# Kernel optimization log

Measured on AMD Instinct MI355X. Metric: run time of the kernel, lower is better.

Reference implementation:

```python
import jax, jax.numpy as jnp
import numpy as np

N = 100000
D = 128
E = 1600000
NEG_SLOPE = 0.2


def gatv2_layer(x, src, dst, Wl, Wr, att, b):
    # GATv2Conv (heads=1, eval mode): lin_l -> source/message feats, lin_r -> target feats
    xl = x @ Wl                      # [N, D]
    xr = x @ Wr                      # [N, D]
    # per-edge score: a^T LeakyReLU(x_l[src] + x_r[dst])
    z = jax.nn.leaky_relu(xl[src] + xr[dst], NEG_SLOPE)  # [E, D]
    e = z @ att                      # [E]
    # segment softmax over incoming edges of each dst node
    m = jax.ops.segment_max(e, dst, num_segments=N)      # [N]
    ex = jnp.exp(e - m[dst])
    s = jax.ops.segment_sum(ex, dst, num_segments=N)     # [N]
    alpha = ex / (s[dst] + 1e-16)                        # [E]
    # weighted scatter-aggregate of source messages
    out = jax.ops.segment_sum(alpha[:, None] * xl[src], dst, num_segments=N)
    return out + b


def setup_inputs() -> dict:
    key = jax.random.key(0)
    ks = jax.random.split(key, 6)
    scale = 1.0 / np.sqrt(D)
    x = jax.random.normal(ks[0], (N, D), dtype=jnp.float32)
    edge_index = jax.random.randint(ks[1], (2, E), 0, N, dtype=jnp.int64)
    Wl = jax.random.normal(ks[2], (3, D, D), dtype=jnp.float32) * scale
    Wr = jax.random.normal(ks[3], (3, D, D), dtype=jnp.float32) * scale
    att = jax.random.normal(ks[4], (3, D), dtype=jnp.float32) * scale
    b = jax.random.normal(ks[5], (3, D), dtype=jnp.float32) * 0.01
    return {"x": x, "Wl": Wl, "Wr": Wr, "att": att, "b": b, "edge_index": edge_index}


def reference(x, Wl, Wr, att, b, edge_index):
    src, dst = edge_index[0], edge_index[1]
    h = gatv2_layer(x, src, dst, Wl[0], Wr[0], att[0], b[0])
    h = jax.nn.relu(h)
    h = gatv2_layer(h, src, dst, Wl[1], Wr[1], att[1], b[1])
    h = jax.nn.relu(h)
    h = gatv2_layer(h, src, dst, Wl[2], Wr[2], att[2], b[2])
    return h
```

## Files before the change

kernel.cpp:

```cpp
#include <hip/hip_runtime.h>
#include <math.h>

#define DD 128
#define NEG 0.2f

typedef short short8 __attribute__((ext_vector_type(8)));
typedef float f32x4 __attribute__((ext_vector_type(4)));
typedef float f32x2 __attribute__((ext_vector_type(2)));
typedef _Float16 h2v __attribute__((ext_vector_type(2)));

__device__ __forceinline__ unsigned short f2bf(float f) {
    unsigned u = __float_as_uint(f);
    return (unsigned short)((u + 0x7fffu + ((u >> 16) & 1u)) >> 16);
}
__device__ __forceinline__ float bf2f(unsigned short h) {
    return __uint_as_float(((unsigned)h) << 16);
}

#if __has_builtin(__builtin_amdgcn_exp2f)
#define EXP2F(x) __builtin_amdgcn_exp2f(x)
#else
#define EXP2F(x) exp2f(x)
#endif

__device__ void excl_scan_1024(int* sh, int* aux) {
    __syncthreads();
    int t = threadIdx.x;
    int base = t * 4;
    int a0 = sh[base], a1 = sh[base + 1], a2 = sh[base + 2], a3 = sh[base + 3];
    int s = a0 + a1 + a2 + a3;
    aux[t] = s;
    __syncthreads();
    for (int off = 1; off < 256; off <<= 1) {
        int v = (t >= off) ? aux[t - off] : 0;
        __syncthreads();
        aux[t] += v;
        __syncthreads();
    }
    int excl = aux[t] - s;
    sh[base] = excl;
    sh[base + 1] = excl + a0;
    sh[base + 2] = excl + a0 + a1;
    sh[base + 3] = excl + a0 + a1 + a2;
    __syncthreads();
}

__global__ __launch_bounds__(256) void k_histC(const int* __restrict__ dst,
                                               int* __restrict__ histC, int E, int CB) {
    __shared__ int h[1024];
    int t = threadIdx.x;
    for (int j = t; j < 1024; j += 256) h[j] = 0;
    __syncthreads();
    int stride = gridDim.x * 256;
    for (int i = blockIdx.x * 256 + t; i < E; i += stride)
        atomicAdd(&h[dst[i] >> 7], 1);
    __syncthreads();
    for (int j = t; j < CB; j += 256)
        if (h[j]) atomicAdd(&histC[j], h[j]);
}

__global__ __launch_bounds__(256) void k_scanC2(const int* __restrict__ histC,
                                                int* __restrict__ baseC,
                                                int* __restrict__ cursorC, int CB) {
    __shared__ int sh[1024];
    __shared__ int aux[256];
    int t = threadIdx.x;
    for (int j = t; j < 1024; j += 256) sh[j] = (j < CB) ? histC[j] : 0;
    excl_scan_1024(sh, aux);
    for (int j = t; j <= CB; j += 256) {
        baseC[j] = sh[j];
        if (j < CB) cursorC[j] = sh[j];
    }
}

#define CHUNK 8192
__global__ __launch_bounds__(256) void k_part3(const int* __restrict__ srcI,
                                               const int* __restrict__ dstI,
                                               int* __restrict__ cursorC,
                                               uint2* __restrict__ part,
                                               int E, int CB) {
    __shared__ int sh[1024];
    __shared__ int aux[256];
    __shared__ int resBase[1024];
    __shared__ int cur[1024];
    __shared__ uint2 stage[CHUNK];
    int t = threadIdx.x;
    int c0 = blockIdx.x * CHUNK;
    int cnt = E - c0; if (cnt > CHUNK) cnt = CHUNK;

    for (int j = t; j < 1024; j += 256) sh[j] = 0;
    __syncthreads();
    for (int i = t; i < cnt; i += 256)
        atomicAdd(&sh[dstI[c0 + i] >> 7], 1);
    __syncthreads();
    for (int j = t; j < CB; j += 256) {
        int c = sh[j];
        resBase[j] = c ? atomicAdd(&cursorC[j], c) : 0;
    }
    excl_scan_1024(sh, aux);
    for (int j = t; j < 1024; j += 256) cur[j] = sh[j];
    __syncthreads();
    for (int i = t; i < cnt; i += 256) {
        unsigned s = (unsigned)srcI[c0 + i];
        unsigned d = (unsigned)dstI[c0 + i];
        int b = (int)(d >> 7);
        int pos = atomicAdd(&cur[b], 1);
        stage[pos].x = s;
        stage[pos].y = d;
    }
    __syncthreads();
    for (int i = t; i < cnt; i += 256) {
        uint2 v = stage[i];
        int b = (int)(v.y >> 7);
        part[resBase[b] + (i - sh[b])] = v;
    }
}

__global__ __launch_bounds__(256) void k_part4(const uint2* __restrict__ part,
                                               const int* __restrict__ baseC,
                                               int* __restrict__ srcs,
                                               int* __restrict__ row_ptr,
                                               int N) {
    __shared__ int hist[128];
    __shared__ int incl[128];
    __shared__ int cur[128];
    __shared__ unsigned srcS[8192];
    int b = blockIdx.x;
    int t = threadIdx.x;
    int base = baseC[b];
    int cnt = baseC[b + 1] - base;
    int node0 = b << 7;

    if (t < 128) hist[t] = 0;
    __syncthreads();
    for (int i = t; i < cnt; i += 256)
        atomicAdd(&hist[part[base + i].y & 127], 1);
    __syncthreads();
    if (t < 128) incl[t] = hist[t];
    __syncthreads();
    for (int off = 1; off < 128; off <<= 1) {
        int v = 0;
        if (t < 128 && t >= off) v = incl[t - off];
        __syncthreads();
        if (t < 128) incl[t] += v;
        __syncthreads();
    }
    if (t < 128) cur[t] = incl[t] - hist[t];
    __syncthreads();
    for (int i = t; i < cnt; i += 256) {
        uint2 e = part[base + i];
        int r = atomicAdd(&cur[e.y & 127], 1);
        if (r < 8192) srcS[r] = e.x;
    }
    __syncthreads();
    for (int i = t; i < cnt; i += 256)
        srcs[base + i] = (int)srcS[i];
    int nodes = N - node0; if (nodes > 128) nodes = 128;
    if (t < nodes) row_ptr[node0 + t + 1] = base + incl[t];
    if (b == 0 && t == 0) row_ptr[0] = 0;
}

#define NCH 8192
__global__ __launch_bounds__(256) void k_deghist(const int* __restrict__ row_ptr,
                                                 int* __restrict__ histD, int N) {
    __shared__ int h[128];
    int t = threadIdx.x;
    if (t < 128) h[t] = 0;
    __syncthreads();
    int c0 = blockIdx.x * NCH;
    int cnt = N - c0; if (cnt > NCH) cnt = NCH;
    for (int i = t; i < cnt; i += 256) {
        int deg = row_ptr[c0 + i + 1] - row_ptr[c0 + i];
        int c = deg < 127 ? deg : 127;
        atomicAdd(&h[c], 1);
    }
    __syncthreads();
    if (t < 128 && h[t]) atomicAdd(&histD[t], h[t]);
}

__global__ __launch_bounds__(128) void k_degscan(const int* __restrict__ histD,
                                                 int* __restrict__ cursorD) {
    __shared__ int sh[128];
    int t = threadIdx.x;
    int v0 = histD[t];
    sh[t] = v0;
    __syncthreads();
    for (int off = 1; off < 128; off <<= 1) {
        int v = (t >= off) ? sh[t - off] : 0;
        __syncthreads();
        sh[t] += v;
        __syncthreads();
    }
    cursorD[t] = sh[t] - v0;
}

__global__ __launch_bounds__(256) void k_degpart(const int* __restrict__ row_ptr,
                                                 int* __restrict__ cursorD,
                                                 int* __restrict__ order, int N) {
    __shared__ int hist[128];
    __shared__ int excl[128];
    __shared__ int cur[128];
    __shared__ int resB[128];
    __shared__ int stage[NCH];
    int t = threadIdx.x;
    int c0 = blockIdx.x * NCH;
    int cnt = N - c0; if (cnt > NCH) cnt = NCH;

    if (t < 128) hist[t] = 0;
    __syncthreads();
    for (int i = t; i < cnt; i += 256) {
        int deg = row_ptr[c0 + i + 1] - row_ptr[c0 + i];
        int c = deg < 127 ? deg : 127;
        atomicAdd(&hist[c], 1);
    }
    __syncthreads();
    if (t < 128) resB[t] = hist[t] ? atomicAdd(&cursorD[t], hist[t]) : 0;
    if (t < 128) excl[t] = hist[t];
    __syncthreads();
    for (int off = 1; off < 128; off <<= 1) {
        int v = 0;
        if (t < 128 && t >= off) v = excl[t - off];
        __syncthreads();
        if (t < 128) excl[t] += v;
        __syncthreads();
    }
    if (t < 128) { excl[t] -= hist[t]; cur[t] = excl[t]; }
    __syncthreads();
    for (int i = t; i < cnt; i += 256) {
        int deg = row_ptr[c0 + i + 1] - row_ptr[c0 + i];
        int c = deg < 127 ? deg : 127;
        int p = atomicAdd(&cur[c], 1);
        stage[p] = (c << 20) | (c0 + i);
    }
    __syncthreads();
    for (int i = t; i < cnt; i += 256) {
        int v = stage[i];
        int c = v >> 20;
        order[resB[c] + (i - excl[c])] = v & 0xFFFFF;
    }
}

__global__ void k_castw(const float* __restrict__ Wl, const float* __restrict__ Wr,
                        unsigned short* __restrict__ Wth, unsigned short* __restrict__ Wtl) {
    int idx = blockIdx.x * blockDim.x + threadIdx.x;
    if (idx >= 3 * 256 * 128) return;
    int L = idx >> 15;
    int rem = idx & 32767;
    int nn = rem >> 7;
    int k = rem & 127;
    float v = (nn < 128) ? Wl[L * 16384 + k * 128 + nn]
                         : Wr[L * 16384 + k * 128 + (nn - 128)];
    unsigned short h = f2bf(v);
    Wth[idx] = h;
    Wtl[idx] = f2bf(v - bf2f(h));
}

__device__ __forceinline__ void cvt8(const float4& a, const float4& b, uint4& hi, uint4& lo) {
    union US8 { unsigned short s[8]; uint4 u; } H, Lo;
    float f[8] = {a.x, a.y, a.z, a.w, b.x, b.y, b.z, b.w};
#pragma unroll
    for (int i = 0; i < 8; i++) {
        unsigned short h = f2bf(f[i]);
        H.s[i] = h;
        Lo.s[i] = f2bf(f[i] - bf2f(h));
    }
    hi = H.u; lo = Lo.u;
}

template <int F32SRC>
__global__ __launch_bounds__(256) void k_gemm(const float* __restrict__ Xf,
                                              const unsigned short* __restrict__ Ahi,
                                              const unsigned short* __restrict__ Alo,
                                              const unsigned short* __restrict__ Wth,
                                              const unsigned short* __restrict__ Wtl,
                                              _Float16* __restrict__ xl, _Float16* __restrict__ xr,
                                              int M, int L, int gX) {
    __shared__ unsigned short sA[2][128][40];
    __shared__ unsigned short sB[2][128][40];
    int b = blockIdx.x;
    int grp = b >> 4, j8 = b & 7, half = (b >> 3) & 1;
    int ry = grp * 8 + j8;
    if (ry >= gX) return;

    int t = threadIdx.x;
    int lane = t & 63;
    int l15 = lane & 15;
    int quad = lane >> 4;
    int wave = t >> 6;
    int wm = wave & 1;
    int wn = wave >> 1;
    int r0 = ry * 128;
    const unsigned short* WthL = Wth + ((size_t)L * 256 + half * 128) * 128;
    const unsigned short* WtlL = Wtl + ((size_t)L * 256 + half * 128) * 128;

    int row0 = t >> 2,       row1 = (t + 256) >> 2;
    int kq   = (t & 3) * 8;
    int gr0 = r0 + row0; gr0 = gr0 < M ? gr0 : M - 1;
    int gr1 = r0 + row1; gr1 = gr1 < M ? gr1 : M - 1;

    uint4 rAh0, rAh1, rAl0, rAl1, rBh0, rBh1, rBl0, rBl1;
    float4 f00, f01, f10, f11;

#define GLOADA(K0)                                                          \
    if (F32SRC) {                                                           \
        f00 = *(const float4*)(Xf + (size_t)gr0 * DD + (K0) + kq);          \
        f01 = *(const float4*)(Xf + (size_t)gr0 * DD + (K0) + kq + 4);      \
        f10 = *(const float4*)(Xf + (size_t)gr1 * DD + (K0) + kq);          \
        f11 = *(const float4*)(Xf + (size_t)gr1 * DD + (K0) + kq + 4);      \
    } else {                                                                \
        rAh0 = *(const uint4*)(Ahi + (size_t)gr0 * DD + (K0) + kq);         \
        rAh1 = *(const uint4*)(Ahi + (size_t)gr1 * DD + (K0) + kq);         \
        rAl0 = *(const uint4*)(Alo + (size_t)gr0 * DD + (K0) + kq);         \
        rAl1 = *(const uint4*)(Alo + (size_t)gr1 * DD + (K0) + kq);         \
    }
#define GLOADB(K0)                                                          \
    rBh0 = *(const uint4*)(WthL + (size_t)row0 * DD + (K0) + kq);           \
    rBh1 = *(const uint4*)(WthL + (size_t)row1 * DD + (K0) + kq);           \
    rBl0 = *(const uint4*)(WtlL + (size_t)row0 * DD + (K0) + kq);           \
    rBl1 = *(const uint4*)(WtlL + (size_t)row1 * DD + (K0) + kq);

    f32x4 acc[4][4] = {};
    union F8 { short8 v; uint4 u; };

    GLOADA(0);
    GLOADB(0);

#pragma unroll
    for (int kc = 0; kc < 4; kc++) {
        if (kc) __syncthreads();
        if (F32SRC) {
            cvt8(f00, f01, rAh0, rAl0);
            cvt8(f10, f11, rAh1, rAl1);
        }
        *(uint4*)&sA[0][row0][kq] = rAh0;
        *(uint4*)&sA[0][row1][kq] = rAh1;
        *(uint4*)&sA[1][row0][kq] = rAl0;
        *(uint4*)&sA[1][row1][kq] = rAl1;
        *(uint4*)&sB[0][row0][kq] = rBh0;
        *(uint4*)&sB[0][row1][kq] = rBh1;
        *(uint4*)&sB[1][row0][kq] = rBl0;
        *(uint4*)&sB[1][row1][kq] = rBl1;
        __syncthreads();
        if (kc < 3) { GLOADA((kc + 1) * 32); GLOADB((kc + 1) * 32); }

        F8 ah[4], al[4], bh[4], bl[4];
#pragma unroll
        for (int mt = 0; mt < 4; mt++) {
            ah[mt].u = *(const uint4*)&sA[0][wm * 64 + mt * 16 + l15][quad * 8];
            al[mt].u = *(const uint4*)&sA[1][wm * 64 + mt * 16 + l15][quad * 8];
        }
#pragma unroll
        for (int nt = 0; nt < 4; nt++) {
            bh[nt].u = *(const uint4*)&sB[0][wn * 64 + nt * 16 + l15][quad * 8];
            bl[nt].u = *(const uint4*)&sB[1][wn * 64 + nt * 16 + l15][quad * 8];
        }
#pragma unroll
        for (int mt = 0; mt < 4; mt++)
#pragma unroll
            for (int nt = 0; nt < 4; nt++) {
                acc[mt][nt] = __builtin_amdgcn_mfma_f32_16x16x32_bf16(ah[mt].v, bh[nt].v, acc[mt][nt], 0, 0, 0);
                acc[mt][nt] = __builtin_amdgcn_mfma_f32_16x16x32_bf16(al[mt].v, bh[nt].v, acc[mt][nt], 0, 0, 0);
                acc[mt][nt] = __builtin_amdgcn_mfma_f32_16x16x32_bf16(ah[mt].v, bl[nt].v, acc[mt][nt], 0, 0, 0);
            }
    }
#undef GLOADA
#undef GLOADB

    _Float16* C = half ? xr : xl;
#pragma unroll
    for (int mt = 0; mt < 4; mt++)
#pragma unroll
        for (int r = 0; r < 4; r++) {
            int row = r0 + wm * 64 + mt * 16 + quad * 4 + r;
            if (row < M) {
#pragma unroll
                for (int nt = 0; nt < 4; nt++)
                    C[(size_t)row * DD + wn * 64 + nt * 16 + l15] = (_Float16)acc[mt][nt][r];
            }
        }
}

__global__ __launch_bounds__(256) void k_attn(const _Float16* __restrict__ xl,
                                              const _Float16* __restrict__ xr,
                                              const int* __restrict__ row_ptr,
                                              const int* __restrict__ srcs,
                                              const int* __restrict__ order,
                                              const float* __restrict__ att,
                                              const float* __restrict__ bias,
                                              float* __restrict__ outF,
                                              unsigned short* __restrict__ outHi,
                                              unsigned short* __restrict__ outLo,
                                              int n, int mode) {
    int wid = (blockIdx.x * blockDim.x + threadIdx.x) >> 6;
    int l = threadIdx.x & 63;
    int l15 = l & 15;
    int g = l >> 4;
    int idx = wid * 4 + g;
    bool act = idx < n;
    int d = act ? order[idx] : 0;

    union Q { uint4 q; h2v h[4]; };
    const float LOG2E = 1.44269504088896f;

    h2v at[4], xrh[4];
    {
        float4 a0 = *(const float4*)(att + l15 * 8);
        float4 a1 = *(const float4*)(att + l15 * 8 + 4);
        at[0] = h2v{(_Float16)(a0.x * LOG2E), (_Float16)(a0.y * LOG2E)};
        at[1] = h2v{(_Float16)(a0.z * LOG2E), (_Float16)(a0.w * LOG2E)};
        at[2] = h2v{(_Float16)(a1.x * LOG2E), (_Float16)(a1.y * LOG2E)};
        at[3] = h2v{(_Float16)(a1.z * LOG2E), (_Float16)(a1.w * LOG2E)};
        Q hr; hr.q = *(const uint4*)(xr + (size_t)d * DD + l15 * 8);
#pragma unroll
        for (int j = 0; j < 4; j++) xrh[j] = hr.h[j];
    }
    const _Float16 cneg = (_Float16)NEG;

    int beg = act ? row_ptr[d] : 0;
    int end = act ? row_ptr[d + 1] : 0;
    int cnt = end - beg;

    int mc = cnt;
    mc = max(mc, __shfl_xor(mc, 16, 64));
    mc = max(mc, __shfl_xor(mc, 32, 64));
    int iters = (mc + 3) >> 2;

    float lse = 0.f;
    float av[8] = {};

    int i0 = beg, i1 = beg + 1, i2 = beg + 2, i3 = beg + 3;
    bool v0 = i0 < end, v1 = i1 < end, v2 = i2 < end, v3 = i3 < end;
    int s0 = v0 ? srcs[i0] : 0;
    int s1 = v1 ? srcs[i1] : 0;
    int s2 = v2 ? srcs[i2] : 0;
    int s3 = v3 ? srcs[i3] : 0;

    const _Float16* xlp = xl + l15 * 8;

    for (int it = 0; it < iters; ++it) {
        Q h0, h1, h2, h3;
        h0.q = *(const uint4*)(xlp + (size_t)s0 * DD);
        h1.q = *(const uint4*)(xlp + (size_t)s1 * DD);
        h2.q = *(const uint4*)(xlp + (size_t)s2 * DD);
        h3.q = *(const uint4*)(xlp + (size_t)s3 * DD);
        int n0 = i0 + 4, n1 = i1 + 4, n2 = i2 + 4, n3 = i3 + 4;
        bool nv0 = n0 < end, nv1 = n1 < end, nv2 = n2 < end, nv3 = n3 < end;
        int t0 = nv0 ? srcs[n0] : 0;
        int t1 = nv1 ? srcs[n1] : 0;
        int t2 = nv2 ? srcs[n2] : 0;
        int t3 = nv3 ? srcs[n3] : 0;

        float p0 = 0.f, p1 = 0.f, p2 = 0.f, p3 = 0.f;
#pragma unroll
        for (int j = 0; j < 4; j++) {
            h2v z0 = h0.h[j] + xrh[j];
            h2v zl0 = __builtin_elementwise_max(z0, z0 * cneg);
            p0 = __builtin_amdgcn_fdot2(zl0, at[j], p0, false);
            h2v z1 = h1.h[j] + xrh[j];
            h2v zl1 = __builtin_elementwise_max(z1, z1 * cneg);
            p1 = __builtin_amdgcn_fdot2(zl1, at[j], p1, false);
            h2v z2 = h2.h[j] + xrh[j];
            h2v zl2 = __builtin_elementwise_max(z2, z2 * cneg);
            p2 = __builtin_amdgcn_fdot2(zl2, at[j], p2, false);
            h2v z3 = h3.h[j] + xrh[j];
            h2v zl3 = __builtin_elementwise_max(z3, z3 * cneg);
            p3 = __builtin_amdgcn_fdot2(zl3, at[j], p3, false);
        }
        p0 += __shfl_xor(p0, 1, 64);  p1 += __shfl_xor(p1, 1, 64);
        p2 += __shfl_xor(p2, 1, 64);  p3 += __shfl_xor(p3, 1, 64);
        p0 += __shfl_xor(p0, 2, 64);  p1 += __shfl_xor(p1, 2, 64);
        p2 += __shfl_xor(p2, 2, 64);  p3 += __shfl_xor(p3, 2, 64);
        p0 += __shfl_xor(p0, 4, 64);  p1 += __shfl_xor(p1, 4, 64);
        p2 += __shfl_xor(p2, 4, 64);  p3 += __shfl_xor(p3, 4, 64);
        p0 += __shfl_xor(p0, 8, 64);  p1 += __shfl_xor(p1, 8, 64);
        p2 += __shfl_xor(p2, 8, 64);  p3 += __shfl_xor(p3, 8, 64);
        p0 = fminf(fmaxf(p0, -86.f), 86.f);
        p1 = fminf(fmaxf(p1, -86.f), 86.f);
        p2 = fminf(fmaxf(p2, -86.f), 86.f);
        p3 = fminf(fmaxf(p3, -86.f), 86.f);
        float w0 = v0 ? EXP2F(p0) : 0.f;
        float w1 = v1 ? EXP2F(p1) : 0.f;
        float w2 = v2 ? EXP2F(p2) : 0.f;
        float w3 = v3 ? EXP2F(p3) : 0.f;
        lse += (w0 + w1) + (w2 + w3);
#pragma unroll
        for (int j = 0; j < 4; j++) {
            av[2 * j]     += (float)h0.h[j][0] * w0;
            av[2 * j + 1] += (float)h0.h[j][1] * w0;
            av[2 * j]     += (float)h1.h[j][0] * w1;
            av[2 * j + 1] += (float)h1.h[j][1] * w1;
            av[2 * j]     += (float)h2.h[j][0] * w2;
            av[2 * j + 1] += (float)h2.h[j][1] * w2;
            av[2 * j]     += (float)h3.h[j][0] * w3;
            av[2 * j + 1] += (float)h3.h[j][1] * w3;
        }
        i0 = n0; i1 = n1; i2 = n2; i3 = n3;
        v0 = nv0; v1 = nv1; v2 = nv2; v3 = nv3;
        s0 = t0; s1 = t1; s2 = t2; s3 = t3;
    }

    if (act) {
        float inv = (cnt > 0) ? 1.0f / lse : 0.f;
        float o[8];
        float4 b0 = *(const float4*)(bias + l15 * 8);
        float4 b1 = *(const float4*)(bias + l15 * 8 + 4);
        float bv[8] = {b0.x, b0.y, b0.z, b0.w, b1.x, b1.y, b1.z, b1.w};
#pragma unroll
        for (int j = 0; j < 8; j++) o[j] = av[j] * inv + bv[j];
        if (mode) {
            union U8 { unsigned short s[8]; uint4 q; };
            U8 hh, ll;
#pragma unroll
            for (int j = 0; j < 8; j++) {
                float v = fmaxf(o[j], 0.f);
                hh.s[j] = f2bf(v);
                ll.s[j] = f2bf(v - bf2f(hh.s[j]));
            }
            *(uint4*)(outHi + (size_t)d * DD + l15 * 8) = hh.q;
            *(uint4*)(outLo + (size_t)d * DD + l15 * 8) = ll.q;
        } else {
            float4 o0 = {o[0], o[1], o[2], o[3]};
            float4 o1 = {o[4], o[5], o[6], o[7]};
            float* op = outF + (size_t)d * DD + l15 * 8;
            *(float4*)op = o0;
            *(float4*)(op + 4) = o1;
        }
    }
}

extern "C" void kernel_launch(void* const* d_in, const int* in_sizes, int n_in,
                              void* d_out, int out_size, void* d_ws, size_t ws_size,
                              hipStream_t stream) {
    const float* x    = (const float*)d_in[0];
    const float* Wl   = (const float*)d_in[1];
    const float* Wr   = (const float*)d_in[2];
    const float* att  = (const float*)d_in[3];
    const float* bias = (const float*)d_in[4];
    const int*   ei   = (const int*)d_in[5];

    int N = in_sizes[0] / DD;
    int E = in_sizes[5] / 2;
    const int* srcI = ei;
    const int* dstI = ei + E;
    float* out = (float*)d_out;
    int CB = (N + 127) >> 7;

    char* ws = (char*)d_ws;
    size_t off = 0;
    auto alloc = [&](size_t bytes) -> void* {
        void* p = ws + off;
        off += (bytes + 255) & ~(size_t)255;
        return p;
    };
    _Float16*       xl   = (_Float16*)alloc((size_t)N * DD * 2);
    _Float16*       xr   = (_Float16*)alloc((size_t)N * DD * 2);
    unsigned short* Ahi  = (unsigned short*)alloc((size_t)N * DD * 2);
    unsigned short* Alo  = (unsigned short*)alloc((size_t)N * DD * 2);
    unsigned short* Wth  = (unsigned short*)alloc((size_t)3 * 256 * 128 * 2);
    unsigned short* Wtl  = (unsigned short*)alloc((size_t)3 * 256 * 128 * 2);
    uint2* part    = (uint2*)alloc((size_t)E * 8);
    int*   srcs    = (int*)alloc((size_t)E * 4);
    int*   row_ptr = (int*)alloc((size_t)(N + 1) * 4);
    int*   order   = (int*)alloc((size_t)N * 4);
    int*   histC   = (int*)alloc((size_t)(CB + 1) * 4);
    int*   baseC   = (int*)alloc((size_t)(CB + 1) * 4);
    int*   cursorC = (int*)alloc((size_t)(CB + 1) * 4);
    int*   histD   = (int*)alloc(128 * 4);
    int*   cursorD = (int*)alloc(128 * 4);

    const int tb = 256;
    (void)hipMemsetAsync(histC, 0, (size_t)CB * 4, stream);
    (void)hipMemsetAsync(histD, 0, 128 * 4, stream);
    k_histC<<<256, 256, 0, stream>>>(dstI, histC, E, CB);
    k_scanC2<<<1, 256, 0, stream>>>(histC, baseC, cursorC, CB);
    k_part3<<<(E + CHUNK - 1) / CHUNK, 256, 0, stream>>>(srcI, dstI, cursorC, part, E, CB);
    k_part4<<<CB, 256, 0, stream>>>(part, baseC, srcs, row_ptr, N);
    int gD = (N + NCH - 1) / NCH;
    k_deghist<<<gD, 256, 0, stream>>>(row_ptr, histD, N);
    k_degscan<<<1, 128, 0, stream>>>(histD, cursorD);
    k_degpart<<<gD, 256, 0, stream>>>(row_ptr, cursorD, order, N);

    k_castw<<<(3 * 256 * 128 + tb - 1) / tb, tb, 0, stream>>>(Wl, Wr, Wth, Wtl);

    int gX = (N + 127) / 128;
    int NB = 16 * ((gX + 7) / 8);
    for (int L = 0; L < 3; ++L) {
        if (L == 0)
            k_gemm<1><<<NB, 256, 0, stream>>>(x, Ahi, Alo, Wth, Wtl, xl, xr, N, L, gX);
        else
            k_gemm<0><<<NB, 256, 0, stream>>>(x, Ahi, Alo, Wth, Wtl, xl, xr, N, L, gX);
        k_attn<<<((size_t)N * 16 + tb - 1) / tb, tb, 0, stream>>>(
            xl, xr, row_ptr, srcs, order, att + (size_t)L * DD, bias + (size_t)L * DD,
            out, Ahi, Alo, N, (L < 2) ? 1 : 0);
    }
}
```

Baseline: 481.3 us.

## Fold scan and weight-cast kernels into neighbouring preprocessing kernels to cut launches

Removes the single-block scan kernels for the coarse-bucket and degree histograms; each partition block now recomputes the exclusive scan of the global histogram redundantly and adds it to an atomic cursor that starts at zero. The weight bf16 split cast is merged into the histogram kernel as extra blocks, and the two memsets become one. This targets launch overhead and serialization gaps from tiny kernels, at the cost of redundant per-block scan work and extra shared memory.

```diff
diff --git a/kernel.cpp b/kernel.cpp
--- a/kernel.cpp
+++ b/kernel.cpp
@@ -46,40 +46,48 @@
 }
 
 __global__ __launch_bounds__(256) void k_histC(const int* __restrict__ dst,
-                                               int* __restrict__ histC, int E, int CB) {
+                                               int* __restrict__ histC, int E, int CB,
+                                               const float* __restrict__ Wl,
+                                               const float* __restrict__ Wr,
+                                               unsigned short* __restrict__ Wth,
+                                               unsigned short* __restrict__ Wtl) {
     __shared__ int h[1024];
     int t = threadIdx.x;
+    if (blockIdx.x >= 256) {
+        int idx = (blockIdx.x - 256) * 256 + t;
+        if (idx < 3 * 256 * 128) {
+            int L = idx >> 15;
+            int rem = idx & 32767;
+            int nn = rem >> 7;
+            int k = rem & 127;
+            float v = (nn < 128) ? Wl[L * 16384 + k * 128 + nn]
+                                 : Wr[L * 16384 + k * 128 + (nn - 128)];
+            unsigned short hh = f2bf(v);
+            Wth[idx] = hh;
+            Wtl[idx] = f2bf(v - bf2f(hh));
+        }
+        return;
+    }
     for (int j = t; j < 1024; j += 256) h[j] = 0;
     __syncthreads();
-    int stride = gridDim.x * 256;
+    int stride = 256 * 256;
     for (int i = blockIdx.x * 256 + t; i < E; i += stride)
         atomicAdd(&h[dst[i] >> 7], 1);
     __syncthreads();
     for (int j = t; j < CB; j += 256)
         if (h[j]) atomicAdd(&histC[j], h[j]);
-}
-
-__global__ __launch_bounds__(256) void k_scanC2(const int* __restrict__ histC,
-                                                int* __restrict__ baseC,
-                                                int* __restrict__ cursorC, int CB) {
-    __shared__ int sh[1024];
-    __shared__ int aux[256];
-    int t = threadIdx.x;
-    for (int j = t; j < 1024; j += 256) sh[j] = (j < CB) ? histC[j] : 0;
-    excl_scan_1024(sh, aux);
-    for (int j = t; j <= CB; j += 256) {
-        baseC[j] = sh[j];
-        if (j < CB) cursorC[j] = sh[j];
-    }
 }
 
 #define CHUNK 8192
 __global__ __launch_bounds__(256) void k_part3(const int* __restrict__ srcI,
                                                const int* __restrict__ dstI,
-                                               int* __restrict__ cursorC,
+                                               const int* __restrict__ histC,
+                                               int* __restrict__ cursor0C,
+                                               int* __restrict__ baseC,
                                                uint2* __restrict__ part,
                                                int E, int CB) {
     __shared__ int sh[1024];
+    __shared__ int gsh[1024];
     __shared__ int aux[256];
     __shared__ int resBase[1024];
     __shared__ int cur[1024];
@@ -89,14 +97,17 @@
     int cnt = E - c0; if (cnt > CHUNK) cnt = CHUNK;
 
     for (int j = t; j < 1024; j += 256) sh[j] = 0;
+    for (int j = t; j < 1024; j += 256) gsh[j] = (j < CB) ? histC[j] : 0;
     __syncthreads();
     for (int i = t; i < cnt; i += 256)
         atomicAdd(&sh[dstI[c0 + i] >> 7], 1);
-    __syncthreads();
+    excl_scan_1024(gsh, aux);
     for (int j = t; j < CB; j += 256) {
         int c = sh[j];
-        resBase[j] = c ? atomicAdd(&cursorC[j], c) : 0;
-    }
+        resBase[j] = gsh[j] + (c ? atomicAdd(&cursor0C[j], c) : 0);
+    }
+    if (blockIdx.x == 0)
+        for (int j = t; j <= CB; j += 256) baseC[j] = gsh[j];
     excl_scan_1024(sh, aux);
     for (int j = t; j < 1024; j += 256) cur[j] = sh[j];
     __syncthreads();
@@ -178,26 +189,12 @@
     if (t < 128 && h[t]) atomicAdd(&histD[t], h[t]);
 }
 
-__global__ __launch_bounds__(128) void k_degscan(const int* __restrict__ histD,
-                                                 int* __restrict__ cursorD) {
-    __shared__ int sh[128];
-    int t = threadIdx.x;
-    int v0 = histD[t];
-    sh[t] = v0;
-    __syncthreads();
-    for (int off = 1; off < 128; off <<= 1) {
-        int v = (t >= off) ? sh[t - off] : 0;
-        __syncthreads();
-        sh[t] += v;
-        __syncthreads();
-    }
-    cursorD[t] = sh[t] - v0;
-}
-
 __global__ __launch_bounds__(256) void k_degpart(const int* __restrict__ row_ptr,
-                                                 int* __restrict__ cursorD,
+                                                 const int* __restrict__ histD,
+                                                 int* __restrict__ cursor0D,
                                                  int* __restrict__ order, int N) {
     __shared__ int hist[128];
+    __shared__ int gex[128];
     __shared__ int excl[128];
     __shared__ int cur[128];
     __shared__ int resB[128];
@@ -206,7 +203,8 @@
     int c0 = blockIdx.x * NCH;
     int cnt = N - c0; if (cnt > NCH) cnt = NCH;
 
-    if (t < 128) hist[t] = 0;
+    int g0 = 0;
+    if (t < 128) { hist[t] = 0; g0 = histD[t]; gex[t] = g0; }
     __syncthreads();
     for (int i = t; i < cnt; i += 256) {
         int deg = row_ptr[c0 + i + 1] - row_ptr[c0 + i];
@@ -214,7 +212,14 @@
         atomicAdd(&hist[c], 1);
     }
     __syncthreads();
-    if (t < 128) resB[t] = hist[t] ? atomicAdd(&cursorD[t], hist[t]) : 0;
+    for (int off = 1; off < 128; off <<= 1) {
+        int v = 0;
+        if (t < 128 && t >= off) v = gex[t - off];
+        __syncthreads();
+        if (t < 128) gex[t] += v;
+        __syncthreads();
+    }
+    if (t < 128) resB[t] = (gex[t] - g0) + (hist[t] ? atomicAdd(&cursor0D[t], hist[t]) : 0);
     if (t < 128) excl[t] = hist[t];
     __syncthreads();
     for (int off = 1; off < 128; off <<= 1) {
@@ -238,21 +243,6 @@
         int c = v >> 20;
         order[resB[c] + (i - excl[c])] = v & 0xFFFFF;
     }
-}
-
-__global__ void k_castw(const float* __restrict__ Wl, const float* __restrict__ Wr,
-                        unsigned short* __restrict__ Wth, unsigned short* __restrict__ Wtl) {
-    int idx = blockIdx.x * blockDim.x + threadIdx.x;
-    if (idx >= 3 * 256 * 128) return;
-    int L = idx >> 15;
-    int rem = idx & 32767;
-    int nn = rem >> 7;
-    int k = rem & 127;
-    float v = (nn < 128) ? Wl[L * 16384 + k * 128 + nn]
-                         : Wr[L * 16384 + k * 128 + (nn - 128)];
-    unsigned short h = f2bf(v);
-    Wth[idx] = h;
-    Wtl[idx] = f2bf(v - bf2f(h));
 }
 
 __device__ __forceinline__ void cvt8(const float4& a, const float4& b, uint4& hi, uint4& lo) {
@@ -562,25 +552,22 @@
     int*   srcs    = (int*)alloc((size_t)E * 4);
     int*   row_ptr = (int*)alloc((size_t)(N + 1) * 4);
     int*   order   = (int*)alloc((size_t)N * 4);
-    int*   histC   = (int*)alloc((size_t)(CB + 1) * 4);
     int*   baseC   = (int*)alloc((size_t)(CB + 1) * 4);
-    int*   cursorC = (int*)alloc((size_t)(CB + 1) * 4);
-    int*   histD   = (int*)alloc(128 * 4);
-    int*   cursorD = (int*)alloc(128 * 4);
+    int*   z       = (int*)alloc((size_t)(2 * CB + 256) * 4);
+    int*   histC    = z;
+    int*   cursor0C = z + CB;
+    int*   histD    = z + 2 * CB;
+    int*   cursor0D = z + 2 * CB + 128;
 
     const int tb = 256;
-    (void)hipMemsetAsync(histC, 0, (size_t)CB * 4, stream);
-    (void)hipMemsetAsync(histD, 0, 128 * 4, stream);
-    k_histC<<<256, 256, 0, stream>>>(dstI, histC, E, CB);
-    k_scanC2<<<1, 256, 0, stream>>>(histC, baseC, cursorC, CB);
-    k_part3<<<(E + CHUNK - 1) / CHUNK, 256, 0, stream>>>(srcI, dstI, cursorC, part, E, CB);
+    (void)hipMemsetAsync(z, 0, (size_t)(2 * CB + 256) * 4, stream);
+    k_histC<<<640, 256, 0, stream>>>(dstI, histC, E, CB, Wl, Wr, Wth, Wtl);
+    k_part3<<<(E + CHUNK - 1) / CHUNK, 256, 0, stream>>>(srcI, dstI, histC, cursor0C,
+                                                         baseC, part, E, CB);
     k_part4<<<CB, 256, 0, stream>>>(part, baseC, srcs, row_ptr, N);
     int gD = (N + NCH - 1) / NCH;
     k_deghist<<<gD, 256, 0, stream>>>(row_ptr, histD, N);
-    k_degscan<<<1, 128, 0, stream>>>(histD, cursorD);
-    k_degpart<<<gD, 256, 0, stream>>>(row_ptr, cursorD, order, N);
-
-    k_castw<<<(3 * 256 * 128 + tb - 1) / tb, tb, 0, stream>>>(Wl, Wr, Wth, Wtl);
+    k_degpart<<<gD, 256, 0, stream>>>(row_ptr, histD, cursor0D, order, N);
 
     int gX = (N + 127) / 128;
     int NB = 16 * ((gX + 7) / 8);
```

After: 477.9 us. No clear change (-0.7%).
